# Kernel tuning notes

Measured on AMD Instinct MI355X. Metric: run time of the kernel, lower is better.

## Reference

```python
import jax, jax.numpy as jnp
import numpy as np

HIDDEN = 1024
HEADS = 16
HEAD_DIM = HIDDEN // HEADS
FF = 4 * HIDDEN
B, S = 2, 2048


def _linear_params(key, out_dim, in_dim):
    kw, kb = jax.random.split(key)
    bound = 1.0 / np.sqrt(in_dim)
    W = jax.random.uniform(kw, (out_dim, in_dim), jnp.float32, -bound, bound)
    b = jax.random.uniform(kb, (out_dim,), jnp.float32, -bound, bound)
    return W, b


def setup_inputs() -> dict:
    key = jax.random.key(0)
    ks = jax.random.split(key, 8)
    x = jax.random.normal(ks[0], (B, S, HIDDEN), jnp.float32)
    attention_mask = jnp.ones((B, S), jnp.float32)
    Wq, bq = _linear_params(ks[1], HIDDEN, HIDDEN)
    Wk, bk = _linear_params(ks[2], HIDDEN, HIDDEN)
    Wv, bv = _linear_params(ks[3], HIDDEN, HIDDEN)
    Wo, bo = _linear_params(ks[4], HIDDEN, HIDDEN)
    W1, b1 = _linear_params(ks[5], FF, HIDDEN)
    W2, b2 = _linear_params(ks[6], HIDDEN, FF)
    g1 = jnp.ones((HIDDEN,), jnp.float32); be1 = jnp.zeros((HIDDEN,), jnp.float32)
    g2 = jnp.ones((HIDDEN,), jnp.float32); be2 = jnp.zeros((HIDDEN,), jnp.float32)
    return dict(x=x, attention_mask=attention_mask,
                Wq=Wq, bq=bq, Wk=Wk, bk=bk, Wv=Wv, bv=bv, Wo=Wo, bo=bo,
                W1=W1, b1=b1, W2=W2, b2=b2,
                g1=g1, be1=be1, g2=g2, be2=be2)


def _layer_norm(x, g, b, eps=1e-5):
    mu = jnp.mean(x, axis=-1, keepdims=True)
    var = jnp.mean(jnp.square(x - mu), axis=-1, keepdims=True)
    return (x - mu) * jax.lax.rsqrt(var + eps) * g + b


def reference(x, attention_mask, Wq, bq, Wk, bk, Wv, bv, Wo, bo,
              W1, b1, W2, b2, g1, be1, g2, be2):
    # Dropout is identity (eval mode / deterministic reference).
    residual = x
    h = _layer_norm(x, g1, be1)
    # [B,S,H] -> [B,nH,S,dh]
    def heads(t):
        return t.reshape(B, S, HEADS, HEAD_DIM).transpose(0, 2, 1, 3)
    q = heads(h @ Wq.T + bq)
    k = heads(h @ Wk.T + bk)
    v = heads(h @ Wv.T + bv)
    scores = jnp.einsum('bhqd,bhkd->bhqk', q, k) / np.sqrt(HEAD_DIM).astype(np.float32)
    scores = scores + (attention_mask[:, None, None, :] - 1.0) * 10000.0
    attn = jax.nn.softmax(scores, axis=-1)
    ctx = jnp.einsum('bhqk,bhkd->bhqd', attn, v)
    ctx = ctx.transpose(0, 2, 1, 3).reshape(B, S, HIDDEN)
    attn_out = ctx @ Wo.T + bo
    x = residual + attn_out
    residual = x
    h = _layer_norm(x, g2, be2)
    h = jax.nn.gelu(h @ W1.T + b1, approximate=False)
    h = h @ W2.T + b2
    return residual + h
```

## Files before the change

kernel.cpp:

```cpp
#include <hip/hip_runtime.h>
#include <hip/hip_bf16.h>
#include <math.h>

typedef __bf16 bf16;
typedef __bf16 bf16x4v __attribute__((ext_vector_type(4)));
typedef __bf16 bf16x8 __attribute__((ext_vector_type(8)));
typedef float  f32x4  __attribute__((ext_vector_type(4)));

#define HIDDEN 1024
#define TOKENS 4096
#define FFDIM  4096
#define SEQ    2048
#define NHEAD  16

#define LOG2E 1.44269504088896340736f

__device__ __forceinline__ void async_copy16(bf16* lds, const bf16* g)
{
    __builtin_amdgcn_global_load_lds(
        (__attribute__((address_space(1))) void*)g,
        (__attribute__((address_space(3))) void*)lds,
        16, 0, 0);
}

__global__ __launch_bounds__(256) void cvt_all_kernel(const float* __restrict__ wq,
    const float* __restrict__ wk, const float* __restrict__ wv, const float* __restrict__ wo,
    const float* __restrict__ w1, const float* __restrict__ w2, bf16* __restrict__ out)
{
    size_t i = ((size_t)blockIdx.x * 256 + threadIdx.x) * 4;
    int sel = (int)(i >> 20);
    const float* src;
    size_t off;
    if (sel < 4) { src = (sel == 0) ? wq : (sel == 1) ? wk : (sel == 2) ? wv : wo; off = i & ((1u << 20) - 1); }
    else if (sel < 8) { src = w1; off = i - ((size_t)4 << 20); }
    else              { src = w2; off = i - ((size_t)8 << 20); }
    float4 v = *(const float4*)&src[off];
    bf16x4v o = { (bf16)v.x, (bf16)v.y, (bf16)v.z, (bf16)v.w };
    *(bf16x4v*)&out[i] = o;
}

__global__ __launch_bounds__(256) void concat_bias_kernel(const float* __restrict__ bq,
    const float* __restrict__ bk, const float* __restrict__ bv, float* __restrict__ o)
{
    int i = blockIdx.x * 256 + threadIdx.x;
    float v = (i < 1024) ? bq[i] : (i < 2048 ? bk[i - 1024] : bv[i - 2048]);
    o[i] = v;
}

__global__ __launch_bounds__(256) void ln_kernel(const float* __restrict__ in,
    const float* __restrict__ g, const float* __restrict__ be, bf16* __restrict__ out)
{
    int row = blockIdx.x;
    int tid = threadIdx.x;
    const float* x = in + (size_t)row * HIDDEN;
    int i0 = tid * 4;
    float4 v = *(const float4*)&x[i0];
    float s  = v.x + v.y + v.z + v.w;
    float s2 = v.x*v.x + v.y*v.y + v.z*v.z + v.w*v.w;
    #pragma unroll
    for (int off = 32; off > 0; off >>= 1) { s += __shfl_xor(s, off); s2 += __shfl_xor(s2, off); }
    __shared__ float red[2][4];
    int wave = tid >> 6;
    if ((tid & 63) == 0) { red[0][wave] = s; red[1][wave] = s2; }
    __syncthreads();
    float ts  = red[0][0] + red[0][1] + red[0][2] + red[0][3];
    float ts2 = red[1][0] + red[1][1] + red[1][2] + red[1][3];
    float mu   = ts  * (1.0f / HIDDEN);
    float var  = ts2 * (1.0f / HIDDEN) - mu * mu;
    float rstd = rsqrtf(var + 1e-5f);
    float4 gg = *(const float4*)&g[i0];
    float4 bb = *(const float4*)&be[i0];
    bf16x4v o;
    o[0] = (bf16)((v.x - mu) * rstd * gg.x + bb.x);
    o[1] = (bf16)((v.y - mu) * rstd * gg.y + bb.y);
    o[2] = (bf16)((v.z - mu) * rstd * gg.z + bb.z);
    o[3] = (bf16)((v.w - mu) * rstd * gg.w + bb.w);
    *(bf16x4v*)&out[(size_t)row * HIDDEN + i0] = o;
}

template<int BM, int EPI, typename OT>
__global__ __launch_bounds__(256) void gemm_bt(const bf16* __restrict__ A, const bf16* __restrict__ Bt,
    const float* __restrict__ bias, const float* __restrict__ res, OT* __restrict__ C,
    int M, int N, int K)
{
    constexpr int MT = BM / 32;
    __shared__ bf16 As[BM * 64];
    __shared__ bf16 Bs[128 * 64];
    int tid  = threadIdx.x;
    int wave = tid >> 6, lane = tid & 63;
    int lm = lane & 15, quad = lane >> 4;
    int m0 = blockIdx.x * BM, n0 = blockIdx.y * 128;
    int wm = (wave >> 1) * (MT * 16), wn = (wave & 1) * 64;
    int r8 = lane >> 3, c8 = lane & 7;
    int gsw = (c8 ^ (r8 & 7)) * 8;
    f32x4 acc[MT][4] = {};
    for (int k0 = 0; k0 < K; k0 += 64) {
        #pragma unroll
        for (int ch = wave; ch < BM / 8; ch += 4)
            async_copy16(As + ch * 512, &A[(size_t)(m0 + ch * 8 + r8) * K + k0 + gsw]);
        #pragma unroll
        for (int ch = wave; ch < 16; ch += 4)
            async_copy16(Bs + ch * 512, &Bt[(size_t)(n0 + ch * 8 + r8) * K + k0 + gsw]);
        __syncthreads();
        bf16x8 af[MT][2], bfr[4][2];
        #pragma unroll
        for (int ks = 0; ks < 2; ks++) {
            int co = ((ks * 4 + quad) ^ (lm & 7)) * 8;
            #pragma unroll
            for (int t = 0; t < MT; t++) af[t][ks]  = *(const bf16x8*)&As[(wm + t * 16 + lm) * 64 + co];
            #pragma unroll
            for (int t = 0; t < 4; t++)  bfr[t][ks] = *(const bf16x8*)&Bs[(wn + t * 16 + lm) * 64 + co];
        }
        #pragma unroll
        for (int mt = 0; mt < MT; mt++)
            #pragma unroll
            for (int nt = 0; nt < 4; nt++)
                #pragma unroll
                for (int ks = 0; ks < 2; ks++)
                    acc[mt][nt] = __builtin_amdgcn_mfma_f32_16x16x32_bf16(af[mt][ks], bfr[nt][ks], acc[mt][nt], 0, 0, 0);
        __syncthreads();
    }
    #pragma unroll
    for (int mt = 0; mt < MT; mt++) {
        #pragma unroll
        for (int nt = 0; nt < 4; nt++) {
            int col = n0 + wn + nt * 16 + lm;
            float bv = bias[col];
            #pragma unroll
            for (int r = 0; r < 4; r++) {
                int row = m0 + wm + mt * 16 + quad * 4 + r;
                float vv = acc[mt][nt][r] + bv;
                if (EPI == 1) vv = 0.5f * vv * (1.0f + erff(vv * 0.70710678118654752f));
                if (EPI == 2) vv += res[(size_t)row * N + col];
                C[(size_t)row * N + col] = (OT)vv;
            }
        }
    }
}

__global__ __launch_bounds__(256) void gemm_qkv(const bf16* __restrict__ A, const bf16* __restrict__ W,
    const float* __restrict__ bias, bf16* __restrict__ qb, bf16* __restrict__ kb, bf16* __restrict__ vt)
{
    constexpr int K = HIDDEN;
    __shared__ bf16 As[128 * 64];
    __shared__ bf16 Bs[128 * 64];
    int tid  = threadIdx.x;
    int wave = tid >> 6, lane = tid & 63;
    int lm = lane & 15, quad = lane >> 4;
    int m0 = blockIdx.x * 128, n0 = blockIdx.y * 128;
    int wm = (wave >> 1) * 64, wn = (wave & 1) * 64;
    int r8 = lane >> 3, c8 = lane & 7;
    int gsw = (c8 ^ (r8 & 7)) * 8;
    f32x4 acc[4][4] = {};
    for (int k0 = 0; k0 < K; k0 += 64) {
        #pragma unroll
        for (int ch = wave; ch < 16; ch += 4) {
            async_copy16(As + ch * 512, &A[(size_t)(m0 + ch * 8 + r8) * K + k0 + gsw]);
            async_copy16(Bs + ch * 512, &W[(size_t)(n0 + ch * 8 + r8) * K + k0 + gsw]);
        }
        __syncthreads();
        bf16x8 af[4][2], bfr[4][2];
        #pragma unroll
        for (int ks = 0; ks < 2; ks++) {
            int co = ((ks * 4 + quad) ^ (lm & 7)) * 8;
            #pragma unroll
            for (int t = 0; t < 4; t++) {
                af[t][ks]  = *(const bf16x8*)&As[(wm + t * 16 + lm) * 64 + co];
                bfr[t][ks] = *(const bf16x8*)&Bs[(wn + t * 16 + lm) * 64 + co];
            }
        }
        #pragma unroll
        for (int mt = 0; mt < 4; mt++)
            #pragma unroll
            for (int nt = 0; nt < 4; nt++)
                #pragma unroll
                for (int ks = 0; ks < 2; ks++)
                    acc[mt][nt] = __builtin_amdgcn_mfma_f32_16x16x32_bf16(af[mt][ks], bfr[nt][ks], acc[mt][nt], 0, 0, 0);
        __syncthreads();
    }
    int region = n0 >> 10;
    #pragma unroll
    for (int mt = 0; mt < 4; mt++) {
        #pragma unroll
        for (int nt = 0; nt < 4; nt++) {
            int col = n0 + wn + nt * 16 + lm;
            float bv = bias[col];
            int cl = col & 1023;
            #pragma unroll
            for (int r = 0; r < 4; r++) {
                int row = m0 + wm + mt * 16 + quad * 4 + r;
                float vv = acc[mt][nt][r] + bv;
                if (region == 0)      qb[(size_t)row * HIDDEN + cl] = (bf16)vv;
                else if (region == 1) kb[(size_t)row * HIDDEN + cl] = (bf16)vv;
                else {
                    int h = cl >> 6, d = cl & 63;
                    int b = row >> 11, s = row & 2047;
                    vt[(((size_t)(b * NHEAD + h)) * 64 + d) * SEQ + s] = (bf16)vv;
                }
            }
        }
    }
}

__global__ __launch_bounds__(512) void attn_kernel(const bf16* __restrict__ Q, const bf16* __restrict__ K,
    const bf16* __restrict__ Vt, const float* __restrict__ mask, bf16* __restrict__ O)
{
    __shared__ bf16 Ks[2][64 * 64];
    __shared__ bf16 Vs[2][64 * 64];
    __shared__ bf16 Ps[8][16 * 72];
    int tid = threadIdx.x, wave = tid >> 6, lane = tid & 63;
    int lm = lane & 15, quad = lane >> 4;
    int bh = blockIdx.y, b = bh >> 4, h = bh & 15;
    int q0 = blockIdx.x * 128 + wave * 16;
    const size_t base  = ((size_t)b * SEQ) * HIDDEN + h * 64;
    const size_t vbase = (size_t)bh * 64 * SEQ;
    int srow8 = lane >> 3, spos = lane & 7;
    bf16x8 qf[2];
    #pragma unroll
    for (int ks = 0; ks < 2; ks++)
        qf[ks] = *(const bf16x8*)&Q[base + (size_t)(q0 + lm) * HIDDEN + ks * 32 + quad * 8];
    bf16x8 onesf;
    #pragma unroll
    for (int i = 0; i < 8; i++) onesf[i] = (bf16)1.0f;
    f32x4 o[4] = {};
    f32x4 lacc = {};
    const float c0 = 0.125f * LOG2E;
    const float cmk = 10000.0f * LOG2E;
    const float coff = -(cmk + 16.0f);
    bf16* pw = &Ps[wave][0];
    int r = wave * 8 + srow8;
    int gc = spos ^ (r & 7);
    auto stage = [&](int buf, int kt) {
        async_copy16(&Ks[buf][wave * 512], &K [base  + (size_t)(kt + r) * HIDDEN + gc * 8]);
        async_copy16(&Vs[buf][wave * 512], &Vt[vbase + (size_t)r * SEQ + kt + gc * 8]);
    };
    stage(0, 0);
    for (int ti = 0; ti < SEQ / 64; ti++) {
        __syncthreads();
        if (ti + 1 < SEQ / 64) stage((ti + 1) & 1, (ti + 1) * 64);
        const bf16* ksb = Ks[ti & 1];
        const bf16* vsb = Vs[ti & 1];
        int kt = ti * 64;
        f32x4 st[4] = {};
        #pragma unroll
        for (int nt = 0; nt < 4; nt++) {
            #pragma unroll
            for (int ks = 0; ks < 2; ks++) {
                bf16x8 kf = *(const bf16x8*)&ksb[(nt * 16 + lm) * 64 + (((ks * 4 + quad) ^ (lm & 7)) * 8)];
                st[nt] = __builtin_amdgcn_mfma_f32_16x16x32_bf16(kf, qf[ks], st[nt], 0, 0, 0);
            }
        }
        #pragma unroll
        for (int nt = 0; nt < 4; nt++) {
            float4 mv = *(const float4*)&mask[b * SEQ + kt + nt * 16 + quad * 4];
            float p0 = __builtin_amdgcn_exp2f(st[nt][0] * c0 + (mv.x * cmk + coff));
            float p1 = __builtin_amdgcn_exp2f(st[nt][1] * c0 + (mv.y * cmk + coff));
            float p2 = __builtin_amdgcn_exp2f(st[nt][2] * c0 + (mv.z * cmk + coff));
            float p3 = __builtin_amdgcn_exp2f(st[nt][3] * c0 + (mv.w * cmk + coff));
            bf16x4v pk = { (bf16)p0, (bf16)p1, (bf16)p2, (bf16)p3 };
            *(bf16x4v*)&pw[lm * 72 + nt * 16 + quad * 4] = pk;
        }
        bf16x8 pf[2];
        #pragma unroll
        for (int ks = 0; ks < 2; ks++)
            pf[ks] = *(const bf16x8*)&pw[lm * 72 + ks * 32 + quad * 8];
        lacc = __builtin_amdgcn_mfma_f32_16x16x32_bf16(pf[0], onesf, lacc, 0, 0, 0);
        lacc = __builtin_amdgcn_mfma_f32_16x16x32_bf16(pf[1], onesf, lacc, 0, 0, 0);
        #pragma unroll
        for (int dt = 0; dt < 4; dt++) {
            #pragma unroll
            for (int ks = 0; ks < 2; ks++) {
                bf16x8 vf = *(const bf16x8*)&vsb[(dt * 16 + lm) * 64 + (((ks * 4 + quad) ^ (lm & 7)) * 8)];
                o[dt] = __builtin_amdgcn_mfma_f32_16x16x32_bf16(pf[ks], vf, o[dt], 0, 0, 0);
            }
        }
    }
    #pragma unroll
    for (int rr = 0; rr < 4; rr++) {
        float inv = 1.0f / lacc[rr];
        #pragma unroll
        for (int dt = 0; dt < 4; dt++) {
            float val = o[dt][rr] * inv;
            O[base + (size_t)(q0 + quad * 4 + rr) * HIDDEN + dt * 16 + lm] = (bf16)val;
        }
    }
}

extern "C" void kernel_launch(void* const* d_in, const int* in_sizes, int n_in,
                              void* d_out, int out_size, void* d_ws, size_t ws_size,
                              hipStream_t stream)
{
    (void)in_sizes; (void)n_in; (void)out_size; (void)ws_size;
    const float* x    = (const float*)d_in[0];
    const float* mask = (const float*)d_in[1];
    const float* Wq   = (const float*)d_in[2];
    const float* bq   = (const float*)d_in[3];
    const float* Wk   = (const float*)d_in[4];
    const float* bk   = (const float*)d_in[5];
    const float* Wv   = (const float*)d_in[6];
    const float* bv   = (const float*)d_in[7];
    const float* Wo   = (const float*)d_in[8];
    const float* bo   = (const float*)d_in[9];
    const float* W1   = (const float*)d_in[10];
    const float* b1   = (const float*)d_in[11];
    const float* W2   = (const float*)d_in[12];
    const float* b2   = (const float*)d_in[13];
    const float* g1   = (const float*)d_in[14];
    const float* be1  = (const float*)d_in[15];
    const float* g2   = (const float*)d_in[16];
    const float* be2  = (const float*)d_in[17];
    float* out = (float*)d_out;

    const size_t M1 = 1024u * 1024u;
    bf16* ws    = (bf16*)d_ws;
    bf16* Wqkv_b = ws;
    bf16* Wo_b  = ws + 3 * M1;
    bf16* W1_b  = ws + 4 * M1;
    bf16* W2_b  = ws + 8 * M1;
    bf16* qb    = ws + 12 * M1;
    bf16* kb    = ws + 16 * M1;
    bf16* vt    = ws + 20 * M1;
    bf16* cx    = ws + 24 * M1;
    bf16* h     = ws + 28 * M1;
    bf16* ffb   = ws + 12 * M1;
    float* biasqkv = (float*)(ws + 24 * M1);

    cvt_all_kernel<<<dim3(12288), 256, 0, stream>>>(Wq, Wk, Wv, Wo, W1, W2, Wqkv_b);
    concat_bias_kernel<<<dim3(12), 256, 0, stream>>>(bq, bk, bv, biasqkv);

    ln_kernel<<<dim3(TOKENS), 256, 0, stream>>>(x, g1, be1, h);
    gemm_qkv<<<dim3(32, 24), 256, 0, stream>>>(h, Wqkv_b, biasqkv, qb, kb, vt);
    attn_kernel<<<dim3(SEQ / 128, 32), 512, 0, stream>>>(qb, kb, vt, mask, cx);
    gemm_bt<64, 2, float><<<dim3(64, 8), 256, 0, stream>>>(cx, Wo_b, bo, x, out, TOKENS, HIDDEN, HIDDEN);
    ln_kernel<<<dim3(TOKENS), 256, 0, stream>>>(out, g2, be2, h);
    gemm_bt<128, 1, bf16><<<dim3(32, 32), 256, 0, stream>>>(h, W1_b, b1, nullptr, ffb, TOKENS, FFDIM, HIDDEN);
    gemm_bt<64, 2, float><<<dim3(64, 8), 256, 0, stream>>>(ffb, W2_b, b2, out, out, TOKENS, HIDDEN, FFDIM);
}
```

Baseline: 384.3 us.

## Split attention key tiles across wave pairs and reduce partials via LDS

Each query block of 16 rows is now handled by a pair of waves, and each wave processes half of every 64-key tile. Partial outputs and row sums are combined through shared memory at the end. Block count doubles (64 queries per block), which raises occupancy and parallelism for the attention kernel. It also adds a launch-bounds occupancy hint and an XOR-swizzled P scratch layout. The trade-off is that each block loads K/V tiles for half as many queries, so K/V traffic and staging cost double, plus an extra reduction step.

```diff
diff --git a/kernel.cpp b/kernel.cpp
--- a/kernel.cpp
+++ b/kernel.cpp
@@ -202,17 +202,21 @@
     }
 }
 
-__global__ __launch_bounds__(512) void attn_kernel(const bf16* __restrict__ Q, const bf16* __restrict__ K,
+__global__ __launch_bounds__(512, 8) void attn_kernel(const bf16* __restrict__ Q, const bf16* __restrict__ K,
     const bf16* __restrict__ Vt, const float* __restrict__ mask, bf16* __restrict__ O)
 {
-    __shared__ bf16 Ks[2][64 * 64];
-    __shared__ bf16 Vs[2][64 * 64];
-    __shared__ bf16 Ps[8][16 * 72];
+    __shared__ bf16 smem[20480];
+    bf16* Ks0 = smem;
+    bf16* Ks1 = smem + 4096;
+    bf16* Vs0 = smem + 8192;
+    bf16* Vs1 = smem + 12288;
+    bf16* Ps  = smem + 16384;
     int tid = threadIdx.x, wave = tid >> 6, lane = tid & 63;
     int lm = lane & 15, quad = lane >> 4;
-    int bh = blockIdx.y, b = bh >> 4, h = bh & 15;
-    int q0 = blockIdx.x * 128 + wave * 16;
-    const size_t base  = ((size_t)b * SEQ) * HIDDEN + h * 64;
+    int pair = wave >> 1, h = wave & 1;
+    int bh = blockIdx.y, b = bh >> 4;
+    int q0 = blockIdx.x * 64 + pair * 16;
+    const size_t base  = ((size_t)b * SEQ) * HIDDEN + (bh & 15) * 64;
     const size_t vbase = (size_t)bh * 64 * SEQ;
     int srow8 = lane >> 3, spos = lane & 7;
     bf16x8 qf[2];
@@ -227,61 +231,74 @@
     const float c0 = 0.125f * LOG2E;
     const float cmk = 10000.0f * LOG2E;
     const float coff = -(cmk + 16.0f);
-    bf16* pw = &Ps[wave][0];
+    bf16* pw = Ps + wave * 512;
     int r = wave * 8 + srow8;
     int gc = spos ^ (r & 7);
-    auto stage = [&](int buf, int kt) {
-        async_copy16(&Ks[buf][wave * 512], &K [base  + (size_t)(kt + r) * HIDDEN + gc * 8]);
-        async_copy16(&Vs[buf][wave * 512], &Vt[vbase + (size_t)r * SEQ + kt + gc * 8]);
+    auto stage = [&](bf16* kd, bf16* vd, int kt) {
+        async_copy16(kd + wave * 512, &K [base  + (size_t)(kt + r) * HIDDEN + gc * 8]);
+        async_copy16(vd + wave * 512, &Vt[vbase + (size_t)r * SEQ + kt + gc * 8]);
     };
-    stage(0, 0);
+    stage(Ks0, Vs0, 0);
+    int kh = h * 32;
     for (int ti = 0; ti < SEQ / 64; ti++) {
         __syncthreads();
-        if (ti + 1 < SEQ / 64) stage((ti + 1) & 1, (ti + 1) * 64);
-        const bf16* ksb = Ks[ti & 1];
-        const bf16* vsb = Vs[ti & 1];
+        const bf16* ksb = (ti & 1) ? Ks1 : Ks0;
+        const bf16* vsb = (ti & 1) ? Vs1 : Vs0;
+        if (ti + 1 < SEQ / 64) {
+            if (ti & 1) stage(Ks0, Vs0, (ti + 1) * 64);
+            else        stage(Ks1, Vs1, (ti + 1) * 64);
+        }
         int kt = ti * 64;
-        f32x4 st[4] = {};
-        #pragma unroll
-        for (int nt = 0; nt < 4; nt++) {
+        f32x4 st[2] = {};
+        #pragma unroll
+        for (int nt = 0; nt < 2; nt++) {
             #pragma unroll
             for (int ks = 0; ks < 2; ks++) {
-                bf16x8 kf = *(const bf16x8*)&ksb[(nt * 16 + lm) * 64 + (((ks * 4 + quad) ^ (lm & 7)) * 8)];
+                bf16x8 kf = *(const bf16x8*)&ksb[(kh + nt * 16 + lm) * 64 + (((ks * 4 + quad) ^ (lm & 7)) * 8)];
                 st[nt] = __builtin_amdgcn_mfma_f32_16x16x32_bf16(kf, qf[ks], st[nt], 0, 0, 0);
             }
         }
         #pragma unroll
-        for (int nt = 0; nt < 4; nt++) {
-            float4 mv = *(const float4*)&mask[b * SEQ + kt + nt * 16 + quad * 4];
+        for (int nt = 0; nt < 2; nt++) {
+            float4 mv = *(const float4*)&mask[b * SEQ + kt + kh + nt * 16 + quad * 4];
             float p0 = __builtin_amdgcn_exp2f(st[nt][0] * c0 + (mv.x * cmk + coff));
             float p1 = __builtin_amdgcn_exp2f(st[nt][1] * c0 + (mv.y * cmk + coff));
             float p2 = __builtin_amdgcn_exp2f(st[nt][2] * c0 + (mv.z * cmk + coff));
             float p3 = __builtin_amdgcn_exp2f(st[nt][3] * c0 + (mv.w * cmk + coff));
             bf16x4v pk = { (bf16)p0, (bf16)p1, (bf16)p2, (bf16)p3 };
-            *(bf16x4v*)&pw[lm * 72 + nt * 16 + quad * 4] = pk;
-        }
-        bf16x8 pf[2];
-        #pragma unroll
-        for (int ks = 0; ks < 2; ks++)
-            pf[ks] = *(const bf16x8*)&pw[lm * 72 + ks * 32 + quad * 8];
-        lacc = __builtin_amdgcn_mfma_f32_16x16x32_bf16(pf[0], onesf, lacc, 0, 0, 0);
-        lacc = __builtin_amdgcn_mfma_f32_16x16x32_bf16(pf[1], onesf, lacc, 0, 0, 0);
+            *(bf16x4v*)&pw[lm * 32 + (((2 * nt + (quad >> 1)) ^ (lm & 3)) << 3) + ((quad & 1) << 2)] = pk;
+        }
+        bf16x8 pf = *(const bf16x8*)&pw[lm * 32 + ((quad ^ (lm & 3)) << 3)];
+        lacc = __builtin_amdgcn_mfma_f32_16x16x32_bf16(pf, onesf, lacc, 0, 0, 0);
         #pragma unroll
         for (int dt = 0; dt < 4; dt++) {
-            #pragma unroll
-            for (int ks = 0; ks < 2; ks++) {
-                bf16x8 vf = *(const bf16x8*)&vsb[(dt * 16 + lm) * 64 + (((ks * 4 + quad) ^ (lm & 7)) * 8)];
-                o[dt] = __builtin_amdgcn_mfma_f32_16x16x32_bf16(pf[ks], vf, o[dt], 0, 0, 0);
-            }
-        }
-    }
-    #pragma unroll
-    for (int rr = 0; rr < 4; rr++) {
-        float inv = 1.0f / lacc[rr];
-        #pragma unroll
-        for (int dt = 0; dt < 4; dt++) {
-            float val = o[dt][rr] * inv;
-            O[base + (size_t)(q0 + quad * 4 + rr) * HIDDEN + dt * 16 + lm] = (bf16)val;
+            bf16x8 vf = *(const bf16x8*)&vsb[(dt * 16 + lm) * 64 + (((4 * h + quad) ^ (lm & 7)) * 8)];
+            o[dt] = __builtin_amdgcn_mfma_f32_16x16x32_bf16(pf, vf, o[dt], 0, 0, 0);
+        }
+    }
+    __syncthreads();
+    float* scratch = (float*)smem;
+    if (h == 1) {
+        float* s = scratch + ((size_t)pair * 64 + lane) * 20;
+        #pragma unroll
+        for (int dt = 0; dt < 4; dt++) *(f32x4*)&s[dt * 4] = o[dt];
+        *(f32x4*)&s[16] = lacc;
+    }
+    __syncthreads();
+    if (h == 0) {
+        const float* s = scratch + ((size_t)pair * 64 + lane) * 20;
+        f32x4 po[4], pl;
+        #pragma unroll
+        for (int dt = 0; dt < 4; dt++) po[dt] = *(const f32x4*)&s[dt * 4];
+        pl = *(const f32x4*)&s[16];
+        #pragma unroll
+        for (int rr = 0; rr < 4; rr++) {
+            float inv = 1.0f / (lacc[rr] + pl[rr]);
+            #pragma unroll
+            for (int dt = 0; dt < 4; dt++) {
+                float val = (o[dt][rr] + po[dt][rr]) * inv;
+                O[base + (size_t)(q0 + quad * 4 + rr) * HIDDEN + dt * 16 + lm] = (bf16)val;
+            }
         }
     }
 }
@@ -330,7 +347,7 @@
 
     ln_kernel<<<dim3(TOKENS), 256, 0, stream>>>(x, g1, be1, h);
     gemm_qkv<<<dim3(32, 24), 256, 0, stream>>>(h, Wqkv_b, biasqkv, qb, kb, vt);
-    attn_kernel<<<dim3(SEQ / 128, 32), 512, 0, stream>>>(qb, kb, vt, mask, cx);
+    attn_kernel<<<dim3(SEQ / 64, 32), 512, 0, stream>>>(qb, kb, vt, mask, cx);
     gemm_bt<64, 2, float><<<dim3(64, 8), 256, 0, stream>>>(cx, Wo_b, bo, x, out, TOKENS, HIDDEN, HIDDEN);
     ln_kernel<<<dim3(TOKENS), 256, 0, stream>>>(out, g2, be2, h);
     gemm_bt<128, 1, bf16><<<dim3(32, 32), 256, 0, stream>>>(h, W1_b, b1, nullptr, ffb, TOKENS, FFDIM, HIDDEN);
```

After: 389.6 us. No clear change (+1.4%).
